# Kernel optimization log

Hardware: AMD Instinct MI355X
Metric: run time of the kernel (lower is better)

The kernel has to match this reference:

```python
import jax, jax.numpy as jnp
import numpy as np

IM = 128          # imSize
LEAKY_SLOPE = 0.2 # LeakyReLU(0.2) in embed

# FFT / IFFT modules in the original repo (models/fft_utils.py) are
# torch.fft(x, 2, normalized=True) / torch.ifft(x, 2, normalized=True)
# on (N,H,W,2) re/im pairs -> orthonormal 2D (i)FFT of the complex image.

def _forward(x, mask, conv_w):
    # x: (bz, C, H, W); channels 0,1 = real/imag, channels 2: = 'others'
    bz, C, H, W = x.shape
    img = x[:, 0] + 1j * x[:, 1]                      # (bz, H, W) complex
    kspace = jnp.fft.fft2(img, norm='ortho')          # FFT module
    # seperate_mask keeps only k-space row i in copy i -> one-hot over H.
    eye = jnp.eye(IM, dtype=kspace.dtype)             # (IM, H)
    masked = kspace[:, None, :, :] * eye[None, :, :, None]   # (bz, IM, H, W)
    # batched 2D IFFT of each single-row k-space, then magnitude (norm over re/im)
    sep = jnp.abs(jnp.fft.ifft2(masked, norm='ortho')).astype(x.dtype)  # (bz, IM, H, W)
    # embed: 1x1 conv (IM->IM channels, no bias) + LeakyReLU(0.2)
    emb = jnp.einsum('oc,bchw->bohw', conv_w, sep)
    emb = jnp.where(emb >= 0, emb, LEAKY_SLOPE * emb)
    if C > 2:
        return jnp.concatenate([emb, x[:, 2:]], axis=1)  # (bz, IM + C-2, H, W)
    return emb


def setup_inputs() -> dict:
    key = jax.random.key(0)
    k1, k2, k3 = jax.random.split(key, 3)
    x = jax.random.normal(k1, (8, 3, IM, IM), dtype=jnp.float32)
    mask = jax.random.uniform(k2, (8, 1, IM, IM), dtype=jnp.float32)  # unused by forward (API fidelity)
    conv_w = jax.random.normal(k3, (IM, IM), dtype=jnp.float32) / np.sqrt(IM)
    return {"x": x, "mask": mask, "conv_w": conv_w}


def reference(x, mask, conv_w):
    return _forward(x, mask, conv_w)
```

## Files before the change

### kernel.cpp

```cpp
#include <hip/hip_runtime.h>
#include <math.h>

#define IM 128

typedef float f4 __attribute__((ext_vector_type(4)));

__global__ __launch_bounds__(IM) void dft_conv_kernel(const float* __restrict__ x,
                                                      const float* __restrict__ cw,
                                                      float* __restrict__ E) {
    const int blk = blockIdx.x;
    const int b   = blk >> 7;
    const int col = blk & 127;
    const int tid = threadIdx.x;

    __shared__ float2 data_s[IM];
    __shared__ float  mag_s[IM];

    const float* xr = x + (size_t)(b * 3 + 0) * IM * IM;
    const float* xi = x + (size_t)(b * 3 + 1) * IM * IM;
    float2 d;
    d.x = xr[tid * IM + col];
    d.y = xi[tid * IM + col];
    data_s[tid] = d;

    const float ang = (float)(2.0 * M_PI / IM) * (float)tid;
    float sn, cb;
    __sincosf(ang, &sn, &cb);
    const float sb = -sn;
    __syncthreads();

    float c = 1.f, s = 0.f, ar = 0.f, ai = 0.f;
    #pragma unroll 8
    for (int y = 0; y < IM; ++y) {
        const float2 v = data_s[y];
        ar = fmaf(v.x, c, fmaf(-v.y, s, ar));
        ai = fmaf(v.y, c, fmaf( v.x, s, ai));
        const float t0 = s * sb;
        const float t1 = c * sb;
        c = fmaf(c, cb, -t0);
        s = fmaf(s, cb,  t1);
    }
    mag_s[tid] = sqrtf(fmaf(ar, ar, ai * ai)) * (1.0f / IM);
    __syncthreads();

    const f4* cwo = (const f4*)(cw + (size_t)tid * IM);
    float acc = 0.f;
    #pragma unroll 8
    for (int g = 0; g < IM / 4; ++g) {
        const f4 wv = cwo[g];
        acc = fmaf(wv.x, mag_s[4 * g + 0], acc);
        acc = fmaf(wv.y, mag_s[4 * g + 1], acc);
        acc = fmaf(wv.z, mag_s[4 * g + 2], acc);
        acc = fmaf(wv.w, mag_s[4 * g + 3], acc);
    }
    acc = acc >= 0.f ? acc : 0.2f * acc;
    E[((size_t)b * IM + tid) * IM + col] = acc;
}

__global__ __launch_bounds__(256) void bcast_kernel(const f4* __restrict__ E4,
                                                    const f4* __restrict__ x4,
                                                    f4* __restrict__ out4) {
    const int bid = blockIdx.x;
    const int tid = threadIdx.x;
    if (bid < 1024) {
        const int b  = bid >> 7;
        const int o  = bid & 127;
        const int w4 = tid & 31;
        const int hb = tid >> 5;
        const f4 e = E4[(size_t)(b * 128 + o) * 32 + w4];
        f4* dst = out4 + ((size_t)(b * 129 + o) * 128) * 32 + hb * 32 + w4;
        #pragma unroll 16
        for (int k = 0; k < 16; ++k) {
            dst[k * 256] = e;
        }
    } else {
        const int b = bid - 1024;
        const f4* src = x4 + (size_t)(b * 3 + 2) * 4096;
        f4* dst = out4 + ((size_t)(b * 129 + 128)) * 4096;
        #pragma unroll 16
        for (int k = 0; k < 16; ++k) {
            const int idx = tid + 256 * k;
            dst[idx] = src[idx];
        }
    }
}

extern "C" void kernel_launch(void* const* d_in, const int* in_sizes, int n_in,
                              void* d_out, int out_size, void* d_ws, size_t ws_size,
                              hipStream_t stream) {
    const float* x  = (const float*)d_in[0];
    const float* cw = (const float*)d_in[2];
    f4* out4 = (f4*)d_out;
    float* E = (float*)d_ws;

    dft_conv_kernel<<<8 * IM, IM, 0, stream>>>(x, cw, E);
    bcast_kernel<<<1024 + 8, 256, 0, stream>>>((const f4*)E, (const f4*)x, out4);
}
```

Measured before the change: 30.44 us.

## Split 128-point DFT with a radix-4 decimation stage and move channel copy

Each column's 128-point DFT is split by first combining the four 32-strided inputs with a radix-4 butterfly into shared memory. Each thread then runs a 32-term recurrence over the sub-sequence picked by its frequency mod 4, which cuts the inner loop length by four. The pass-through copy of the extra input channel moves from the broadcast kernel into extra blocks of the DFT kernel, so it can overlap with DFT work. The cost is an extra shared-memory stage with one more barrier, plus branch divergence between the butterfly variants.

```diff
diff --git a/kernel.cpp b/kernel.cpp
--- a/kernel.cpp
+++ b/kernel.cpp
@@ -7,13 +7,28 @@
 
 __global__ __launch_bounds__(IM) void dft_conv_kernel(const float* __restrict__ x,
                                                       const float* __restrict__ cw,
-                                                      float* __restrict__ E) {
+                                                      float* __restrict__ E,
+                                                      f4* __restrict__ out4) {
     const int blk = blockIdx.x;
+    const int tid = threadIdx.x;
+
+    if (blk >= 1024) {
+        const int b = blk - 1024;
+        const f4* src = (const f4*)x + (size_t)(b * 3 + 2) * 4096;
+        f4* dst = out4 + ((size_t)(b * 129 + 128)) * 4096;
+        #pragma unroll 8
+        for (int k = 0; k < 32; ++k) {
+            const int idx = tid + IM * k;
+            dst[idx] = src[idx];
+        }
+        return;
+    }
+
     const int b   = blk >> 7;
     const int col = blk & 127;
-    const int tid = threadIdx.x;
 
     __shared__ float2 data_s[IM];
+    __shared__ float2 u4[4][33];
     __shared__ float  mag_s[IM];
 
     const float* xr = x + (size_t)(b * 3 + 0) * IM * IM;
@@ -22,17 +37,43 @@
     d.x = xr[tid * IM + col];
     d.y = xi[tid * IM + col];
     data_s[tid] = d;
+    __syncthreads();
+
+    {
+        const int p = tid >> 5;
+        const int y = tid & 31;
+        const float2 a0 = data_s[y];
+        const float2 a1 = data_s[y + 32];
+        const float2 a2 = data_s[y + 64];
+        const float2 a3 = data_s[y + 96];
+        float2 u;
+        if (p == 0) {
+            u.x = a0.x + a1.x + a2.x + a3.x;
+            u.y = a0.y + a1.y + a2.y + a3.y;
+        } else if (p == 1) {
+            u.x = (a0.x - a2.x) + (a1.y - a3.y);
+            u.y = (a0.y - a2.y) - (a1.x - a3.x);
+        } else if (p == 2) {
+            u.x = a0.x - a1.x + a2.x - a3.x;
+            u.y = a0.y - a1.y + a2.y - a3.y;
+        } else {
+            u.x = (a0.x - a2.x) - (a1.y - a3.y);
+            u.y = (a0.y - a2.y) + (a1.x - a3.x);
+        }
+        u4[p][y] = u;
+    }
+    __syncthreads();
 
     const float ang = (float)(2.0 * M_PI / IM) * (float)tid;
     float sn, cb;
     __sincosf(ang, &sn, &cb);
     const float sb = -sn;
-    __syncthreads();
 
+    const float2* up = u4[tid & 3];
     float c = 1.f, s = 0.f, ar = 0.f, ai = 0.f;
-    #pragma unroll 8
-    for (int y = 0; y < IM; ++y) {
-        const float2 v = data_s[y];
+    #pragma unroll
+    for (int y = 0; y < 32; ++y) {
+        const float2 v = up[y];
         ar = fmaf(v.x, c, fmaf(-v.y, s, ar));
         ai = fmaf(v.y, c, fmaf( v.x, s, ai));
         const float t0 = s * sb;
@@ -58,30 +99,18 @@
 }
 
 __global__ __launch_bounds__(256) void bcast_kernel(const f4* __restrict__ E4,
-                                                    const f4* __restrict__ x4,
                                                     f4* __restrict__ out4) {
     const int bid = blockIdx.x;
     const int tid = threadIdx.x;
-    if (bid < 1024) {
-        const int b  = bid >> 7;
-        const int o  = bid & 127;
-        const int w4 = tid & 31;
-        const int hb = tid >> 5;
-        const f4 e = E4[(size_t)(b * 128 + o) * 32 + w4];
-        f4* dst = out4 + ((size_t)(b * 129 + o) * 128) * 32 + hb * 32 + w4;
-        #pragma unroll 16
-        for (int k = 0; k < 16; ++k) {
-            dst[k * 256] = e;
-        }
-    } else {
-        const int b = bid - 1024;
-        const f4* src = x4 + (size_t)(b * 3 + 2) * 4096;
-        f4* dst = out4 + ((size_t)(b * 129 + 128)) * 4096;
-        #pragma unroll 16
-        for (int k = 0; k < 16; ++k) {
-            const int idx = tid + 256 * k;
-            dst[idx] = src[idx];
-        }
+    const int b  = bid >> 7;
+    const int o  = bid & 127;
+    const int w4 = tid & 31;
+    const int hb = tid >> 5;
+    const f4 e = E4[(size_t)(b * 128 + o) * 32 + w4];
+    f4* dst = out4 + ((size_t)(b * 129 + o) * 128) * 32 + hb * 32 + w4;
+    #pragma unroll 16
+    for (int k = 0; k < 16; ++k) {
+        dst[k * 256] = e;
     }
 }
 
@@ -93,6 +122,6 @@
     f4* out4 = (f4*)d_out;
     float* E = (float*)d_ws;
 
-    dft_conv_kernel<<<8 * IM, IM, 0, stream>>>(x, cw, E);
-    bcast_kernel<<<1024 + 8, 256, 0, stream>>>((const f4*)E, (const f4*)x, out4);
+    dft_conv_kernel<<<1024 + 8, IM, 0, stream>>>(x, cw, E, out4);
+    bcast_kernel<<<1024, 256, 0, stream>>>((const f4*)E, out4);
 }
```

Result: faster. 28.88 us (-5.1%).
